# Optimization experiments

Measured on AMD Instinct MI355X. Metric: run time of the kernel, lower is better.

## Reference

```python
import jax, jax.numpy as jnp
import numpy as np

B, C, N, M_MODES, EMB = 8, 64, 2048, 32, 256
MFREQ = 2 * M_MODES * (2 * M_MODES - 1)  # 4032
SCALE = 1.0 / (C * C)


def setup_inputs() -> dict:
    key = jax.random.key(0)
    ks = jax.random.split(key, 16)
    d = {
        "x": jax.random.normal(ks[0], (B, C, N), jnp.float32),
        "emb": jax.random.normal(ks[1], (B, EMB), jnp.float32),
        "Vf_re": jax.random.normal(ks[2], (MFREQ, N), jnp.float32),
        "Vf_im": jax.random.normal(ks[3], (MFREQ, N), jnp.float32),
        "Vi_re": jax.random.normal(ks[4], (N, MFREQ), jnp.float32),
        "Vi_im": jax.random.normal(ks[5], (N, MFREQ), jnp.float32),
        "w1_re": SCALE * jax.random.uniform(ks[6], (C, C, M_MODES, M_MODES), jnp.float32),
        "w1_im": SCALE * jax.random.uniform(ks[7], (C, C, M_MODES, M_MODES), jnp.float32),
        "w2_re": SCALE * jax.random.uniform(ks[8], (C, C, M_MODES, M_MODES), jnp.float32),
        "w2_im": SCALE * jax.random.uniform(ks[9], (C, C, M_MODES, M_MODES), jnp.float32),
        "m1_re": SCALE * jax.random.uniform(ks[10], (1, M_MODES, M_MODES, EMB), jnp.float32),
        "m1_im": SCALE * jax.random.uniform(ks[11], (1, M_MODES, M_MODES, EMB), jnp.float32),
        "m2_re": SCALE * jax.random.uniform(ks[12], (1, M_MODES, M_MODES, EMB), jnp.float32),
        "m2_im": SCALE * jax.random.uniform(ks[13], (1, M_MODES, M_MODES, EMB), jnp.float32),
    }
    return d


def _spectral_conv(x, emb, Vf, Vi, w1, w2, mod1, mod2):
    m = M_MODES
    # nuft.forward: [B,N,C] complex -> [B,MFREQ,C]
    xc = jnp.transpose(x, (0, 2, 1)).astype(jnp.complex64)
    x_nfft = jnp.einsum('mn,bnc->bmc', Vf, xc)
    # [B,C,2m,2m-1]
    x_ft = jnp.transpose(x_nfft, (0, 2, 1)).reshape(x.shape[0], C, 2 * m, 2 * m - 1)
    embc = emb.astype(jnp.complex64)[:, None, None, :]  # [B,1,1,EMB]
    phi1 = jnp.sum(mod1 * embc, axis=-1)  # [B,m,m]
    phi2 = jnp.sum(mod2 * embc, axis=-1)
    out1 = jnp.einsum('bixy,ioxy->boxy', x_ft[:, :, :m, :m], w1)
    out2 = jnp.einsum('bixy,ioxy->boxy', x_ft[:, :, -m:, :m], w2)
    mod1b = phi1[:, None, :, :] * out1
    mod2b = phi2[:, None, :, :] * out2
    out_ft = jnp.concatenate([mod1b, mod2b], axis=2)  # [B,C,2m,m]
    xf = out_ft.reshape(x.shape[0], C, 2 * m * m)
    # Hermitian-symmetry reconstruction: flip over mode AND channel dims, conj
    xf2 = jnp.conj(jnp.flip(xf[..., 2 * m:], axis=(-2, -1)))
    xf = jnp.concatenate([xf, xf2], axis=-1)  # [B,C,MFREQ]
    xf = jnp.transpose(xf, (0, 2, 1))  # [B,MFREQ,C]
    out = jnp.einsum('nm,bmc->bnc', Vi, xf)  # nuft.inverse -> [B,N,C]
    out = jnp.transpose(out, (0, 2, 1)) / N * 2
    return out.real


def reference(x, emb, Vf_re, Vf_im, Vi_re, Vi_im, w1_re, w1_im, w2_re, w2_im, m1_re, m1_im, m2_re, m2_im):
    Vf = Vf_re + 1j * Vf_im
    Vi = Vi_re + 1j * Vi_im
    w1 = w1_re + 1j * w1_im
    w2 = w2_re + 1j * w2_im
    mod1 = m1_re + 1j * m1_im
    mod2 = m2_re + 1j * m2_im
    return _spectral_conv(x, emb, Vf, Vi, w1, w2, mod1, mod2)
```

## Files before the change

### kernel.cpp

```cpp
#include <hip/hip_runtime.h>

#define BB    8
#define CC    64
#define NN    2048
#define GG    2048
#define MFREQ 4032

typedef __attribute__((ext_vector_type(4))) float f32x4;
typedef __attribute__((ext_vector_type(8))) short bf16x8;

static __device__ __forceinline__ unsigned short f2bf(float f) {
    union { float f; unsigned u; } v; v.f = f;
    unsigned r = v.u + 0x7fff + ((v.u >> 16) & 1);
    return (unsigned short)(r >> 16);
}

#define ASYNC_COPY16(gp, lp)                                                        \
    __builtin_amdgcn_global_load_lds(                                               \
        (const __attribute__((address_space(1))) unsigned int*)(gp),                \
        (__attribute__((address_space(3))) unsigned int*)(lp), 16, 0, 0)

__global__ __launch_bounds__(256) void pack_all(const float* __restrict__ vf_re,
                                                const float* __restrict__ vf_im,
                                                const float* __restrict__ x,
                                                const float* __restrict__ vi_re,
                                                const float* __restrict__ vi_im,
                                                unsigned short* __restrict__ af,
                                                unsigned short* __restrict__ xb,
                                                unsigned short* __restrict__ mi) {
    int blk = blockIdx.x;
    float4 v;
    unsigned short* dst;
    if (blk < 8192) {
        int idx = blk * 256 + threadIdx.x;
        int m = idx >> 9;
        int q = (idx & 511) * 4;
        int g = m & 2047;
        int f = (g >> 5) * 63 + (g & 31);
        const float* src = (m < 2048 ? vf_re : vf_im) + (size_t)f * 2048 + q;
        v = *(const float4*)src;
        dst = af + (size_t)m * 2048 + q;
    } else if (blk < 9216) {
        int idx = (blk - 8192) * 256 + threadIdx.x;
        int q = idx * 4;
        v = *(const float4*)(x + q);
        dst = xb + q;
    } else {
        int idx = (blk - 9216) * 256 + threadIdx.x;
        int n = idx >> 11;
        int q4 = (idx & 2047) * 4;
        int region = q4 >> 11;
        int off = q4 & 2047;
        if (region == 0) {
            v = *(const float4*)(vi_re + (size_t)n * MFREQ + off);
        } else if (region == 1) {
            float4 t = *(const float4*)(vi_im + (size_t)n * MFREQ + off);
            v.x = -t.x; v.y = -t.y; v.z = -t.z; v.w = -t.w;
        } else {
            if (off < 64) { v.x = v.y = v.z = v.w = 0.0f; }
            else {
                const float* src = (region == 2 ? vi_re : vi_im);
                float4 t = *(const float4*)(src + (size_t)n * MFREQ + (4092 - off));
                v.x = t.w; v.y = t.z; v.z = t.y; v.w = t.x;
            }
        }
        dst = mi + (size_t)n * 8192 + q4;
    }
    ushort4 o; o.x = f2bf(v.x); o.y = f2bf(v.y); o.z = f2bf(v.z); o.w = f2bf(v.w);
    *(ushort4*)dst = o;
}

__global__ __launch_bounds__(256) void pack_wt(const float* __restrict__ w1_re,
                                               const float* __restrict__ w1_im,
                                               const float* __restrict__ w2_re,
                                               const float* __restrict__ w2_im,
                                               unsigned int* __restrict__ wt) {
    __shared__ float sre[64][65];
    __shared__ float sim[64][65];
    int wsel = blockIdx.z;
    const float* wre = wsel ? w2_re : w1_re;
    const float* wim = wsel ? w2_im : w1_im;
    int io0 = blockIdx.y * 64, xy0 = blockIdx.x * 64;
    int t = threadIdx.x;
    int r = t >> 2, cq = (t & 3) * 16;
    for (int j = 0; j < 16; j += 4) {
        float4 a = *(const float4*)(wre + (size_t)(io0 + r) * 1024 + xy0 + cq + j);
        float4 b = *(const float4*)(wim + (size_t)(io0 + r) * 1024 + xy0 + cq + j);
        sre[r][cq + j + 0] = a.x; sre[r][cq + j + 1] = a.y; sre[r][cq + j + 2] = a.z; sre[r][cq + j + 3] = a.w;
        sim[r][cq + j + 0] = b.x; sim[r][cq + j + 1] = b.y; sim[r][cq + j + 2] = b.z; sim[r][cq + j + 3] = b.w;
    }
    __syncthreads();
    int iol = t & 63, gq = t >> 6;
    for (int jj = 0; jj < 16; ++jj) {
        int gl = jj * 4 + gq;
        int g = xy0 + gl + wsel * 1024;
        unsigned int o = (unsigned int)f2bf(sre[iol][gl]) | ((unsigned int)f2bf(sim[iol][gl]) << 16);
        wt[(size_t)g * 4096 + io0 + iol] = o;
    }
}

__global__ __launch_bounds__(256) void phi_k(const float* __restrict__ m1_re,
                                             const float* __restrict__ m1_im,
                                             const float* __restrict__ m2_re,
                                             const float* __restrict__ m2_im,
                                             const float* __restrict__ emb,
                                             float* __restrict__ phi_re,
                                             float* __restrict__ phi_im) {
    int g = blockIdx.x, b = blockIdx.y, e = threadIdx.x;
    int xy = g & 1023;
    const float* mr = (g < 1024 ? m1_re : m2_re) + xy * 256;
    const float* mi = (g < 1024 ? m1_im : m2_im) + xy * 256;
    float em = emb[b * 256 + e];
    float pr = mr[e] * em, pi = mi[e] * em;
    __shared__ float sr[4], si[4];
    for (int s = 32; s > 0; s >>= 1) { pr += __shfl_down(pr, s); pi += __shfl_down(pi, s); }
    int wid = e >> 6;
    if ((e & 63) == 0) { sr[wid] = pr; si[wid] = pi; }
    __syncthreads();
    if (e == 0) {
        phi_re[b * 2048 + g] = sr[0] + sr[1] + sr[2] + sr[3];
        phi_im[b * 2048 + g] = si[0] + si[1] + si[2] + si[3];
    }
}

__global__ __launch_bounds__(256, 2) void gemm_sk(const unsigned short* __restrict__ A,
                                                  const unsigned short* __restrict__ Bm,
                                                  float* __restrict__ P,
                                                  int M, int N, int K, int Kper) {
    __shared__ unsigned short As[128 * 64];
    __shared__ unsigned short Bs[128 * 64];
    int t = threadIdx.x;
    int lane = t & 63, w = t >> 6;
    int m0 = blockIdx.y * 128, n0 = blockIdx.x * 128;
    int z = blockIdx.z;
    int kbase = z * Kper;
    int wm = (w >> 1) * 64, wn = (w & 1) * 64;
    int lr = lane & 15, quad = lane >> 4;
    int rsub = lane >> 3, slot = lane & 7;

    f32x4 acc[4][4] = {};

    for (int kk = kbase; kk < kbase + Kper; kk += 64) {
        __syncthreads();
        #pragma unroll
        for (int l = 0; l < 4; ++l) {
            int r = (w * 4 + l) * 8 + rsub;
            int c = slot ^ (r & 7);
            ASYNC_COPY16(A + (size_t)(m0 + r) * K + kk + c * 8, As + r * 64 + slot * 8);
            ASYNC_COPY16(Bm + (size_t)(n0 + r) * K + kk + c * 8, Bs + r * 64 + slot * 8);
        }
        __syncthreads();
        #pragma unroll
        for (int ks = 0; ks < 2; ++ks) {
            bf16x8 af[4], bfr[4];
            #pragma unroll
            for (int i = 0; i < 4; ++i) {
                int row = wm + i * 16 + lr;
                int q = (ks * 4 + quad) ^ (row & 7);
                af[i] = *(const bf16x8*)(As + row * 64 + q * 8);
                int rowb = wn + i * 16 + lr;
                int qb = (ks * 4 + quad) ^ (rowb & 7);
                bfr[i] = *(const bf16x8*)(Bs + rowb * 64 + qb * 8);
            }
            #pragma unroll
            for (int i = 0; i < 4; ++i)
            #pragma unroll
            for (int j = 0; j < 4; ++j)
                acc[i][j] = __builtin_amdgcn_mfma_f32_16x16x32_bf16(af[i], bfr[j], acc[i][j], 0, 0, 0);
        }
    }
    float* Pz = P + (size_t)z * M * N;
    #pragma unroll
    for (int i = 0; i < 4; ++i)
    #pragma unroll
    for (int j = 0; j < 4; ++j) {
        int rr = m0 + wm + i * 16 + quad * 4;
        int cc = n0 + wn + j * 16 + lr;
        float* cp = Pz + (size_t)rr * N + cc;
        f32x4 v = acc[i][j];
        cp[0]             = v.x;
        cp[(size_t)N]     = v.y;
        cp[2 * (size_t)N] = v.z;
        cp[3 * (size_t)N] = v.w;
    }
}

__global__ __launch_bounds__(256) void reduce_k(const float* __restrict__ P,
                                                float* __restrict__ out,
                                                int S, size_t elems, float alpha) {
    size_t idx = ((size_t)blockIdx.x * 256 + threadIdx.x) * 4;
    float4 s = *(const float4*)(P + idx);
    for (int zz = 1; zz < S; ++zz) {
        float4 v = *(const float4*)(P + (size_t)zz * elems + idx);
        s.x += v.x; s.y += v.y; s.z += v.z; s.w += v.w;
    }
    s.x *= alpha; s.y *= alpha; s.z *= alpha; s.w *= alpha;
    *(float4*)(out + idx) = s;
}

__global__ __launch_bounds__(256) void middle_k(const float* __restrict__ O1,
                                                const unsigned int* __restrict__ wt,
                                                const float* __restrict__ phi_re,
                                                const float* __restrict__ phi_im,
                                                unsigned short* __restrict__ Yt) {
    __shared__ unsigned int sW[4096];
    __shared__ float sInc[1024];
    int t = threadIdx.x;
    int g0 = blockIdx.x * 8;
    int b = t >> 5, oo = t & 31;

    unsigned short re0[8], im0[8], re1[8], im1[8];

    #pragma unroll
    for (int gt = 0; gt < 8; ++gt) {
        int g = g0 + gt;
        __syncthreads();
        #pragma unroll
        for (int j = 0; j < 4; ++j)
            ASYNC_COPY16(wt + (size_t)g * 4096 + (j * 256 + t) * 4, sW + (j * 256 + t) * 4);
        {
            const float* src = (t < 128) ? (O1 + (size_t)g * 512 + t * 4)
                                         : (O1 + (size_t)(2048 + g) * 512 + (t - 128) * 4);
            ASYNC_COPY16(src, sInc + t * 4);
        }
        __syncthreads();

        float ar0 = 0.f, ai0 = 0.f, ar1 = 0.f, ai1 = 0.f;
        #pragma unroll 8
        for (int i = 0; i < 64; ++i) {
            float ax = sInc[b * 64 + i];
            float ay = sInc[512 + b * 64 + i];
            unsigned int u0 = sW[i * 64 + oo];
            unsigned int u1 = sW[i * 64 + oo + 32];
            float w0r = __uint_as_float(u0 << 16);
            float w0i = __uint_as_float(u0 & 0xffff0000u);
            float w1r = __uint_as_float(u1 << 16);
            float w1i = __uint_as_float(u1 & 0xffff0000u);
            ar0 += ax * w0r - ay * w0i;  ai0 += ax * w0i + ay * w0r;
            ar1 += ax * w1r - ay * w1i;  ai1 += ax * w1i + ay * w1r;
        }
        float pr = phi_re[b * 2048 + g], pi = phi_im[b * 2048 + g];
        re0[gt] = f2bf(pr * ar0 - pi * ai0);
        im0[gt] = f2bf(pr * ai0 + pi * ar0);
        re1[gt] = f2bf(pr * ar1 - pi * ai1);
        im1[gt] = f2bf(pr * ai1 + pi * ar1);
    }

    uint4 vre0, vim0, vre1, vim1;
    vre0.x = re0[0] | (re0[1] << 16); vre0.y = re0[2] | (re0[3] << 16);
    vre0.z = re0[4] | (re0[5] << 16); vre0.w = re0[6] | (re0[7] << 16);
    vim0.x = im0[0] | (im0[1] << 16); vim0.y = im0[2] | (im0[3] << 16);
    vim0.z = im0[4] | (im0[5] << 16); vim0.w = im0[6] | (im0[7] << 16);
    vre1.x = re1[0] | (re1[1] << 16); vre1.y = re1[2] | (re1[3] << 16);
    vre1.z = re1[4] | (re1[5] << 16); vre1.w = re1[6] | (re1[7] << 16);
    vim1.x = im1[0] | (im1[1] << 16); vim1.y = im1[2] | (im1[3] << 16);
    vim1.z = im1[4] | (im1[5] << 16); vim1.w = im1[6] | (im1[7] << 16);

    {
        size_t r0 = (size_t)(b * 64 + oo) * 8192;
        size_t rf = (size_t)(b * 64 + 63 - oo) * 8192;
        *(uint4*)(Yt + r0 + g0)        = vre0;
        *(uint4*)(Yt + r0 + 2048 + g0) = vim0;
        *(uint4*)(Yt + rf + 4096 + g0) = vre0;
        *(uint4*)(Yt + rf + 6144 + g0) = vim0;
    }
    {
        int o = oo + 32;
        size_t r0 = (size_t)(b * 64 + o) * 8192;
        size_t rf = (size_t)(b * 64 + 63 - o) * 8192;
        *(uint4*)(Yt + r0 + g0)        = vre1;
        *(uint4*)(Yt + r0 + 2048 + g0) = vim1;
        *(uint4*)(Yt + rf + 4096 + g0) = vre1;
        *(uint4*)(Yt + rf + 6144 + g0) = vim1;
    }
}

extern "C" void kernel_launch(void* const* d_in, const int* in_sizes, int n_in,
                              void* d_out, int out_size, void* d_ws, size_t ws_size,
                              hipStream_t stream) {
    const float* x     = (const float*)d_in[0];
    const float* emb   = (const float*)d_in[1];
    const float* vf_re = (const float*)d_in[2];
    const float* vf_im = (const float*)d_in[3];
    const float* vi_re = (const float*)d_in[4];
    const float* vi_im = (const float*)d_in[5];
    const float* w1_re = (const float*)d_in[6];
    const float* w1_im = (const float*)d_in[7];
    const float* w2_re = (const float*)d_in[8];
    const float* w2_im = (const float*)d_in[9];
    const float* m1_re = (const float*)d_in[10];
    const float* m1_im = (const float*)d_in[11];
    const float* m2_re = (const float*)d_in[12];
    const float* m2_im = (const float*)d_in[13];

    char* ws = (char*)d_ws;
    unsigned short* Af = (unsigned short*)(ws);
    unsigned short* Xb = (unsigned short*)(ws + 16777216);
    unsigned short* Mi = (unsigned short*)(ws + 18874368);
    unsigned int*   Wt = (unsigned int*)(ws + 52428800);
    float*          O1 = (float*)(ws + 85983232);
    float*       PhiRe = (float*)(ws + 94371840);
    float*       PhiIm = (float*)(ws + 94437376);
    unsigned short* Yt = (unsigned short*)(ws + 94502912);
    float*          P  = (float*)(ws + 102891520);
    float* out = (float*)d_out;

    pack_all<<<25600, 256, 0, stream>>>(vf_re, vf_im, x, vi_re, vi_im, Af, Xb, Mi);
    pack_wt<<<dim3(16, 64, 2), 256, 0, stream>>>(w1_re, w1_im, w2_re, w2_im, Wt);
    phi_k<<<dim3(2048, 8), 256, 0, stream>>>(m1_re, m1_im, m2_re, m2_im, emb, PhiRe, PhiIm);

    gemm_sk<<<dim3(4, 32, 4), 256, 0, stream>>>(Af, Xb, P, 4096, 512, 2048, 512);
    reduce_k<<<2048, 256, 0, stream>>>(P, O1, 4, (size_t)4096 * 512, 1.0f);

    middle_k<<<256, 256, 0, stream>>>(O1, Wt, PhiRe, PhiIm, Yt);

    gemm_sk<<<dim3(16, 4, 8), 256, 0, stream>>>(Yt, Mi, P, 512, 2048, 8192, 1024);
    reduce_k<<<1024, 256, 0, stream>>>(P, out, 8, (size_t)512 * 2048, 1.0f / 1024.0f);
}
```

Measured before the change: 331.9 us.

## Interleave re/im in first GEMM output and widen middle kernel grid

The first split-K GEMM now writes its partial results with real and imaginary rows interleaved per frequency, so the middle kernel can fetch each (re, im) pair as one float2 and load one contiguous 4 KB slice per frequency. The middle kernel processes 2 frequencies per block instead of 8, giving a 4x larger grid. It prefetches both frequencies' weights into double LDS buffers with a single barrier and has each thread handle two adjacent output channels through uint2 loads. The trade-off is narrower 4-byte stores to Yt instead of 16-byte ones, and more LDS per block.

After: 319.2 us. 1.04x faster.

```diff
diff --git a/kernel.cpp b/kernel.cpp
--- a/kernel.cpp
+++ b/kernel.cpp
@@ -126,7 +126,7 @@
 __global__ __launch_bounds__(256, 2) void gemm_sk(const unsigned short* __restrict__ A,
                                                   const unsigned short* __restrict__ Bm,
                                                   float* __restrict__ P,
-                                                  int M, int N, int K, int Kper) {
+                                                  int M, int N, int K, int Kper, int ilv) {
     __shared__ unsigned short As[128 * 64];
     __shared__ unsigned short Bs[128 * 64];
     int t = threadIdx.x;
@@ -170,18 +170,21 @@
         }
     }
     float* Pz = P + (size_t)z * M * N;
+    size_t rstride = ilv ? 1024 : (size_t)N;
     #pragma unroll
     for (int i = 0; i < 4; ++i)
     #pragma unroll
     for (int j = 0; j < 4; ++j) {
         int rr = m0 + wm + i * 16 + quad * 4;
         int cc = n0 + wn + j * 16 + lr;
-        float* cp = Pz + (size_t)rr * N + cc;
+        size_t base = ilv ? ((size_t)(rr & 2047) * 1024 + cc * 2 + (rr >> 11))
+                          : ((size_t)rr * N + cc);
+        float* cp = Pz + base;
         f32x4 v = acc[i][j];
-        cp[0]             = v.x;
-        cp[(size_t)N]     = v.y;
-        cp[2 * (size_t)N] = v.z;
-        cp[3 * (size_t)N] = v.w;
+        cp[0]           = v.x;
+        cp[rstride]     = v.y;
+        cp[2 * rstride] = v.z;
+        cp[3 * rstride] = v.w;
     }
 }
 
@@ -198,80 +201,64 @@
     *(float4*)(out + idx) = s;
 }
 
-__global__ __launch_bounds__(256) void middle_k(const float* __restrict__ O1,
-                                                const unsigned int* __restrict__ wt,
-                                                const float* __restrict__ phi_re,
-                                                const float* __restrict__ phi_im,
-                                                unsigned short* __restrict__ Yt) {
-    __shared__ unsigned int sW[4096];
-    __shared__ float sInc[1024];
+__global__ __launch_bounds__(256, 4) void middle_k(const float* __restrict__ O1,
+                                                   const unsigned int* __restrict__ wt,
+                                                   const float* __restrict__ phi_re,
+                                                   const float* __restrict__ phi_im,
+                                                   unsigned short* __restrict__ Yt) {
+    __shared__ unsigned int sW[2][4096];
+    __shared__ float sInc[2][1024];
     int t = threadIdx.x;
-    int g0 = blockIdx.x * 8;
-    int b = t >> 5, oo = t & 31;
-
-    unsigned short re0[8], im0[8], re1[8], im1[8];
-
-    #pragma unroll
-    for (int gt = 0; gt < 8; ++gt) {
+    int g0 = blockIdx.x * 2;
+    int b = t >> 5, p = t & 31;
+
+    #pragma unroll
+    for (int gt = 0; gt < 2; ++gt) {
         int g = g0 + gt;
-        __syncthreads();
         #pragma unroll
         for (int j = 0; j < 4; ++j)
-            ASYNC_COPY16(wt + (size_t)g * 4096 + (j * 256 + t) * 4, sW + (j * 256 + t) * 4);
-        {
-            const float* src = (t < 128) ? (O1 + (size_t)g * 512 + t * 4)
-                                         : (O1 + (size_t)(2048 + g) * 512 + (t - 128) * 4);
-            ASYNC_COPY16(src, sInc + t * 4);
-        }
-        __syncthreads();
-
+            ASYNC_COPY16(wt + (size_t)g * 4096 + (j * 256 + t) * 4, &sW[gt][(j * 256 + t) * 4]);
+        ASYNC_COPY16(O1 + (size_t)g * 1024 + t * 4, &sInc[gt][t * 4]);
+    }
+    __syncthreads();
+
+    unsigned short reA[2][2], imA[2][2];
+
+    #pragma unroll
+    for (int gt = 0; gt < 2; ++gt) {
+        int g = g0 + gt;
         float ar0 = 0.f, ai0 = 0.f, ar1 = 0.f, ai1 = 0.f;
+        const float2* incp = (const float2*)sInc[gt] + b * 64;
+        const unsigned int* wp = sW[gt] + 2 * p;
         #pragma unroll 8
         for (int i = 0; i < 64; ++i) {
-            float ax = sInc[b * 64 + i];
-            float ay = sInc[512 + b * 64 + i];
-            unsigned int u0 = sW[i * 64 + oo];
-            unsigned int u1 = sW[i * 64 + oo + 32];
-            float w0r = __uint_as_float(u0 << 16);
-            float w0i = __uint_as_float(u0 & 0xffff0000u);
-            float w1r = __uint_as_float(u1 << 16);
-            float w1i = __uint_as_float(u1 & 0xffff0000u);
-            ar0 += ax * w0r - ay * w0i;  ai0 += ax * w0i + ay * w0r;
-            ar1 += ax * w1r - ay * w1i;  ai1 += ax * w1i + ay * w1r;
+            float2 a = incp[i];
+            uint2 uu = *(const uint2*)(wp + i * 64);
+            float w0r = __uint_as_float(uu.x << 16);
+            float w0i = __uint_as_float(uu.x & 0xffff0000u);
+            float w1r = __uint_as_float(uu.y << 16);
+            float w1i = __uint_as_float(uu.y & 0xffff0000u);
+            ar0 += a.x * w0r - a.y * w0i;  ai0 += a.x * w0i + a.y * w0r;
+            ar1 += a.x * w1r - a.y * w1i;  ai1 += a.x * w1i + a.y * w1r;
         }
         float pr = phi_re[b * 2048 + g], pi = phi_im[b * 2048 + g];
-        re0[gt] = f2bf(pr * ar0 - pi * ai0);
-        im0[gt] = f2bf(pr * ai0 + pi * ar0);
-        re1[gt] = f2bf(pr * ar1 - pi * ai1);
-        im1[gt] = f2bf(pr * ai1 + pi * ar1);
-    }
-
-    uint4 vre0, vim0, vre1, vim1;
-    vre0.x = re0[0] | (re0[1] << 16); vre0.y = re0[2] | (re0[3] << 16);
-    vre0.z = re0[4] | (re0[5] << 16); vre0.w = re0[6] | (re0[7] << 16);
-    vim0.x = im0[0] | (im0[1] << 16); vim0.y = im0[2] | (im0[3] << 16);
-    vim0.z = im0[4] | (im0[5] << 16); vim0.w = im0[6] | (im0[7] << 16);
-    vre1.x = re1[0] | (re1[1] << 16); vre1.y = re1[2] | (re1[3] << 16);
-    vre1.z = re1[4] | (re1[5] << 16); vre1.w = re1[6] | (re1[7] << 16);
-    vim1.x = im1[0] | (im1[1] << 16); vim1.y = im1[2] | (im1[3] << 16);
-    vim1.z = im1[4] | (im1[5] << 16); vim1.w = im1[6] | (im1[7] << 16);
-
-    {
-        size_t r0 = (size_t)(b * 64 + oo) * 8192;
-        size_t rf = (size_t)(b * 64 + 63 - oo) * 8192;
-        *(uint4*)(Yt + r0 + g0)        = vre0;
-        *(uint4*)(Yt + r0 + 2048 + g0) = vim0;
-        *(uint4*)(Yt + rf + 4096 + g0) = vre0;
-        *(uint4*)(Yt + rf + 6144 + g0) = vim0;
-    }
-    {
-        int o = oo + 32;
-        size_t r0 = (size_t)(b * 64 + o) * 8192;
-        size_t rf = (size_t)(b * 64 + 63 - o) * 8192;
-        *(uint4*)(Yt + r0 + g0)        = vre1;
-        *(uint4*)(Yt + r0 + 2048 + g0) = vim1;
-        *(uint4*)(Yt + rf + 4096 + g0) = vre1;
-        *(uint4*)(Yt + rf + 6144 + g0) = vim1;
+        reA[0][gt] = f2bf(pr * ar0 - pi * ai0);
+        imA[0][gt] = f2bf(pr * ai0 + pi * ar0);
+        reA[1][gt] = f2bf(pr * ar1 - pi * ai1);
+        imA[1][gt] = f2bf(pr * ai1 + pi * ar1);
+    }
+
+    #pragma unroll
+    for (int ch = 0; ch < 2; ++ch) {
+        int c = 2 * p + ch;
+        size_t r0 = (size_t)(b * 64 + c) * 8192;
+        size_t rf = (size_t)(b * 64 + 63 - c) * 8192;
+        unsigned int ure = (unsigned int)reA[ch][0] | ((unsigned int)reA[ch][1] << 16);
+        unsigned int uim = (unsigned int)imA[ch][0] | ((unsigned int)imA[ch][1] << 16);
+        *(unsigned int*)(Yt + r0 + g0)        = ure;
+        *(unsigned int*)(Yt + r0 + 2048 + g0) = uim;
+        *(unsigned int*)(Yt + rf + 4096 + g0) = ure;
+        *(unsigned int*)(Yt + rf + 6144 + g0) = uim;
     }
 }
 
@@ -309,11 +296,11 @@
     pack_wt<<<dim3(16, 64, 2), 256, 0, stream>>>(w1_re, w1_im, w2_re, w2_im, Wt);
     phi_k<<<dim3(2048, 8), 256, 0, stream>>>(m1_re, m1_im, m2_re, m2_im, emb, PhiRe, PhiIm);
 
-    gemm_sk<<<dim3(4, 32, 4), 256, 0, stream>>>(Af, Xb, P, 4096, 512, 2048, 512);
+    gemm_sk<<<dim3(4, 32, 4), 256, 0, stream>>>(Af, Xb, P, 4096, 512, 2048, 512, 1);
     reduce_k<<<2048, 256, 0, stream>>>(P, O1, 4, (size_t)4096 * 512, 1.0f);
 
-    middle_k<<<256, 256, 0, stream>>>(O1, Wt, PhiRe, PhiIm, Yt);
-
-    gemm_sk<<<dim3(16, 4, 8), 256, 0, stream>>>(Yt, Mi, P, 512, 2048, 8192, 1024);
+    middle_k<<<1024, 256, 0, stream>>>(O1, Wt, PhiRe, PhiIm, Yt);
+
+    gemm_sk<<<dim3(16, 4, 8), 256, 0, stream>>>(Yt, Mi, P, 512, 2048, 8192, 1024, 0);
     reduce_k<<<1024, 256, 0, stream>>>(P, out, 8, (size_t)512 * 2048, 1.0f / 1024.0f);
 }
```
